# Kernel tuning notes

Measured on AMD Instinct MI355X. Metric: run time of the kernel, lower is better.

## Reference

```python
import jax, jax.numpy as jnp
import numpy as np


def setup_inputs() -> dict:
    key = jax.random.key(0)
    k1, k2, k3, k4 = jax.random.split(key, 4)
    B, T, C, H = 4, 2048, 1024, 64
    x = jax.random.normal(k1, (B, T, C), dtype=jnp.float32)
    # Linear(embed_dim, head_size, bias=False) weights, stored as [C, H] for x @ W
    s = 1.0 / np.sqrt(C)
    Wq = jax.random.normal(k2, (C, H), dtype=jnp.float32) * s
    Wk = jax.random.normal(k3, (C, H), dtype=jnp.float32) * s
    Wv = jax.random.normal(k4, (C, H), dtype=jnp.float32) * s
    return {"x": x, "Wq": Wq, "Wk": Wk, "Wv": Wv}


def reference(x, Wq, Wk, Wv):
    B, T, C = x.shape
    q = x @ Wq  # [B, T, H]
    k = x @ Wk
    v = x @ Wv
    # NOTE: original scales by embed_dim**-0.5 (C), not head_size**-0.5
    scale = C ** (-0.5)
    wei = jnp.einsum("bqh,bkh->bqk", q, k) * scale  # [B, T, T]
    causal = jnp.tril(jnp.ones((T, T), dtype=bool))
    wei = jnp.where(causal, wei, -jnp.inf)
    wei = jax.nn.softmax(wei, axis=-1)
    # dropout_rate = 0 -> identity
    out = jnp.einsum("bqk,bkh->bqh", wei, v)  # [B, T, H]
    return out
```

## Files before the change

### kernel.cpp

```cpp
#include <hip/hip_runtime.h>
#include <hip/hip_bf16.h>
#include <cmath>

#define B_ 4
#define T_ 2048
#define C_ 1024
#define H_ 64
#define K2_ 0.04508422003f
#define THRRAW_ 177.0f
#define NEG_ -3.0e38f

typedef __attribute__((ext_vector_type(4))) float f32x4;
typedef __attribute__((ext_vector_type(8))) short s16x8;
typedef __attribute__((ext_vector_type(4))) unsigned short u16x4;
typedef __attribute__((ext_vector_type(8))) unsigned short u16x8;

__device__ inline unsigned short f2bf(float f) {
    union { __hip_bfloat16 h; unsigned short u; } cv;
    cv.h = __float2bfloat16(f);
    return cv.u;
}

#define LDK 72

__global__ __launch_bounds__(256) void wprep(
    const float* __restrict__ Wq, const float* __restrict__ Wk,
    const float* __restrict__ Wv, unsigned short* __restrict__ wt)
{
    const int g = blockIdx.x * 256 + threadIdx.x;
    const int c = g >> 7;
    const int kg = (g & 127) * 8;
    const float* W = (c < 64) ? Wq : (c < 128) ? Wk : Wv;
    const int col = c & 63;
    u16x4 a, b;
    a.x = f2bf(W[(size_t)(kg + 0) * H_ + col]);
    a.y = f2bf(W[(size_t)(kg + 1) * H_ + col]);
    a.z = f2bf(W[(size_t)(kg + 2) * H_ + col]);
    a.w = f2bf(W[(size_t)(kg + 3) * H_ + col]);
    b.x = f2bf(W[(size_t)(kg + 4) * H_ + col]);
    b.y = f2bf(W[(size_t)(kg + 5) * H_ + col]);
    b.z = f2bf(W[(size_t)(kg + 6) * H_ + col]);
    b.w = f2bf(W[(size_t)(kg + 7) * H_ + col]);
    *(u16x4*)&wt[(size_t)c * C_ + kg] = a;
    *(u16x4*)&wt[(size_t)c * C_ + kg + 4] = b;
}

__global__ __launch_bounds__(256, 4) void proj_dbuf(
    const float* __restrict__ x, const unsigned short* __restrict__ wt,
    unsigned short* __restrict__ qb, unsigned short* __restrict__ kb,
    unsigned short* __restrict__ vt)
{
    __shared__ alignas(16) unsigned short As[2][64 * LDK];
    __shared__ alignas(16) unsigned short Bs[2][64 * LDK];

    const int t = threadIdx.x, lane = t & 63, w = t >> 6;
    const int blk = blockIdx.x;
    const int mat = blk % 3;
    const int row0 = (blk / 3) * 64;
    const int wr = (w >> 1) * 32, wc = (w & 1) * 32;
    const int fr = lane & 15, ko = (lane >> 4) * 8;

    const int ar0 = t >> 4, akc = (t & 15) * 4;
    const int bc0 = t >> 3, bkc = (t & 7) * 8;

    const float* xp = x + (size_t)(row0 + ar0) * C_ + akc;
    const unsigned short* wp = wt + (size_t)(mat * 64 + bc0) * C_ + bkc;

    f32x4 pa[4];
    u16x8 pb[2];

    #pragma unroll
    for (int i = 0; i < 4; ++i) pa[i] = *(const f32x4*)(xp + (size_t)i * 16 * C_);
    #pragma unroll
    for (int i = 0; i < 2; ++i) pb[i] = *(const u16x8*)(wp + (size_t)i * 32 * C_);
    #pragma unroll
    for (int i = 0; i < 4; ++i) {
        u16x4 bv;
        bv.x = f2bf(pa[i].x); bv.y = f2bf(pa[i].y);
        bv.z = f2bf(pa[i].z); bv.w = f2bf(pa[i].w);
        *(u16x4*)&As[0][(ar0 + i * 16) * LDK + akc] = bv;
    }
    #pragma unroll
    for (int i = 0; i < 2; ++i)
        *(u16x8*)&Bs[0][(bc0 + i * 32) * LDK + bkc] = pb[i];

    f32x4 acc[2][2];
    #pragma unroll
    for (int mi = 0; mi < 2; ++mi)
        #pragma unroll
        for (int ni = 0; ni < 2; ++ni)
            acc[mi][ni] = (f32x4){0.f, 0.f, 0.f, 0.f};

    for (int it = 0; it < 16; ++it) {
        __syncthreads();
        const int cur = it & 1;
        if (it < 15) {
            const float* xn = xp + (it + 1) * 64;
            const unsigned short* wn = wp + (it + 1) * 64;
            #pragma unroll
            for (int i = 0; i < 4; ++i) pa[i] = *(const f32x4*)(xn + (size_t)i * 16 * C_);
            #pragma unroll
            for (int i = 0; i < 2; ++i) pb[i] = *(const u16x8*)(wn + (size_t)i * 32 * C_);
        }
        const unsigned short* A = &As[cur][0];
        const unsigned short* Bb = &Bs[cur][0];
        #pragma unroll
        for (int ks = 0; ks < 2; ++ks) {
            s16x8 a0 = *(const s16x8*)&A[(wr + fr) * LDK + ks * 32 + ko];
            s16x8 a1 = *(const s16x8*)&A[(wr + 16 + fr) * LDK + ks * 32 + ko];
            s16x8 b0 = *(const s16x8*)&Bb[(wc + fr) * LDK + ks * 32 + ko];
            s16x8 b1 = *(const s16x8*)&Bb[(wc + 16 + fr) * LDK + ks * 32 + ko];
            acc[0][0] = __builtin_amdgcn_mfma_f32_16x16x32_bf16(a0, b0, acc[0][0], 0, 0, 0);
            acc[0][1] = __builtin_amdgcn_mfma_f32_16x16x32_bf16(a0, b1, acc[0][1], 0, 0, 0);
            acc[1][0] = __builtin_amdgcn_mfma_f32_16x16x32_bf16(a1, b0, acc[1][0], 0, 0, 0);
            acc[1][1] = __builtin_amdgcn_mfma_f32_16x16x32_bf16(a1, b1, acc[1][1], 0, 0, 0);
        }
        if (it < 15) {
            const int nxt = cur ^ 1;
            #pragma unroll
            for (int i = 0; i < 4; ++i) {
                u16x4 bv;
                bv.x = f2bf(pa[i].x); bv.y = f2bf(pa[i].y);
                bv.z = f2bf(pa[i].z); bv.w = f2bf(pa[i].w);
                *(u16x4*)&As[nxt][(ar0 + i * 16) * LDK + akc] = bv;
            }
            #pragma unroll
            for (int i = 0; i < 2; ++i)
                *(u16x8*)&Bs[nxt][(bc0 + i * 32) * LDK + bkc] = pb[i];
        }
    }

    if (mat < 2) {
        unsigned short* outb = (mat == 0) ? qb : kb;
        #pragma unroll
        for (int mi = 0; mi < 2; ++mi)
            #pragma unroll
            for (int ni = 0; ni < 2; ++ni)
                #pragma unroll
                for (int j = 0; j < 4; ++j) {
                    int row = row0 + wr + mi * 16 + (lane >> 4) * 4 + j;
                    int col = wc + ni * 16 + fr;
                    outb[(size_t)row * H_ + col] = f2bf(acc[mi][ni][j]);
                }
    } else {
        __syncthreads();
        unsigned short* Tr = &As[0][0];
        #pragma unroll
        for (int mi = 0; mi < 2; ++mi)
            #pragma unroll
            for (int ni = 0; ni < 2; ++ni)
                #pragma unroll
                for (int j = 0; j < 4; ++j) {
                    int r = wr + mi * 16 + (lane >> 4) * 4 + j;
                    int cc = wc + ni * 16 + fr;
                    Tr[cc * LDK + r] = f2bf(acc[mi][ni][j]);
                }
        __syncthreads();
        int h = t >> 2, c0 = (t & 3) * 16;
        int bb = row0 >> 11, trow = row0 & 2047;
        s16x8 v0 = *(const s16x8*)&Tr[h * LDK + c0];
        s16x8 v1 = *(const s16x8*)&Tr[h * LDK + c0 + 8];
        size_t dst = (size_t)bb * H_ * T_ + (size_t)h * T_ + trow + c0;
        *(s16x8*)&vt[dst] = v0;
        *(s16x8*)&vt[dst + 8] = v1;
    }
}

__global__ __launch_bounds__(512, 4) void attn_mfma(
    const unsigned short* __restrict__ qb, const unsigned short* __restrict__ kb,
    const unsigned short* __restrict__ vt, float* __restrict__ out)
{
    __shared__ alignas(16) unsigned short Ps[8][1024];
    __shared__ float Os[8][16][68];
    __shared__ float Mm[8][16];
    __shared__ float Ll[8][16];

    const int t = threadIdx.x, lane = t & 63, w = t >> 6;
    const int fr = lane & 15, hi4 = lane >> 4;
    const int blk = blockIdx.x;
    const int b = blk & 3;
    const int qt = 127 - (blk >> 2);
    const int qbase = qt * 16;

    const unsigned short* qp = qb + ((size_t)b * T_ + qbase) * H_;
    const unsigned short* kp = kb + (size_t)b * T_ * H_;
    const unsigned short* vp = vt + (size_t)b * H_ * T_;

    s16x8 qf0 = *(const s16x8*)&qp[fr * H_ + hi4 * 8];
    s16x8 qf1 = *(const s16x8*)&qp[fr * H_ + 32 + hi4 * 8];

    const int nt = (qbase + 79) >> 6;
    const int per = (nt + 7) >> 3;
    const int tb = w * per;
    int te = tb + per; if (te > nt) te = nt;

    float m = NEG_, l = 0.f;
    f32x4 o[4];
    #pragma unroll
    for (int hf = 0; hf < 4; ++hf) o[hf] = (f32x4){0.f, 0.f, 0.f, 0.f};

    unsigned short* P = &Ps[w][0];
    const int swz = (fr & 3) << 4;
    const int qrow = qbase + fr;

    for (int kt = tb; kt < te; ++kt) {
        const int kt0 = kt << 6;

        f32x4 s[4];
        #pragma unroll
        for (int n = 0; n < 4; ++n) {
            const unsigned short* kr = &kp[(size_t)(kt0 + n * 16 + fr) * H_ + hi4 * 8];
            s16x8 kf0 = *(const s16x8*)kr;
            s16x8 kf1 = *(const s16x8*)(kr + 32);
            f32x4 a = (f32x4){0.f, 0.f, 0.f, 0.f};
            a = __builtin_amdgcn_mfma_f32_16x16x32_bf16(kf0, qf0, a, 0, 0, 0);
            a = __builtin_amdgcn_mfma_f32_16x16x32_bf16(kf1, qf1, a, 0, 0, 0);
            s[n] = a;
        }

        s16x8 vf[4][2];
        #pragma unroll
        for (int hf = 0; hf < 4; ++hf) {
            const unsigned short* vr = &vp[(size_t)(hf * 16 + fr) * T_ + kt0 + hi4 * 8];
            vf[hf][0] = *(const s16x8*)vr;
            vf[hf][1] = *(const s16x8*)(vr + 32);
        }

        if (kt0 + 63 > qbase) {
            #pragma unroll
            for (int n = 0; n < 4; ++n)
                #pragma unroll
                for (int j = 0; j < 4; ++j) {
                    int key = kt0 + n * 16 + hi4 * 4 + j;
                    s[n][j] = (key > qrow) ? NEG_ : s[n][j];
                }
        }

        float mxl = fmaxf(fmaxf(fmaxf(fmaxf(s[0][0], s[0][1]), fmaxf(s[0][2], s[0][3])),
                                fmaxf(fmaxf(s[1][0], s[1][1]), fmaxf(s[1][2], s[1][3]))),
                          fmaxf(fmaxf(fmaxf(s[2][0], s[2][1]), fmaxf(s[2][2], s[2][3])),
                                fmaxf(fmaxf(s[3][0], s[3][1]), fmaxf(s[3][2], s[3][3]))));
        if (!__all(mxl - m <= THRRAW_)) {
            float mx = fmaxf(mxl, __shfl_xor(mxl, 16));
            mx = fmaxf(mx, __shfl_xor(mx, 32));
            float mn = fmaxf(m, mx);
            float corr = exp2f((m - mn) * K2_);
            m = mn;
            l *= corr;
            #pragma unroll
            for (int j = 0; j < 4; ++j) {
                float cj = __shfl(corr, (lane & 48) + hi4 * 4 + j);
                o[0][j] *= cj; o[1][j] *= cj; o[2][j] *= cj; o[3][j] *= cj;
            }
        }
        const float nmk = -m * K2_;
        float sum = 0.f;
        #pragma unroll
        for (int n = 0; n < 4; ++n)
            #pragma unroll
            for (int j = 0; j < 4; ++j) {
                float p = exp2f(fmaf(s[n][j], K2_, nmk));
                s[n][j] = p; sum += p;
            }
        sum += __shfl_xor(sum, 16);
        sum += __shfl_xor(sum, 32);
        l += sum;

        #pragma unroll
        for (int n = 0; n < 4; ++n) {
            u16x4 pk;
            pk.x = f2bf(s[n][0]); pk.y = f2bf(s[n][1]);
            pk.z = f2bf(s[n][2]); pk.w = f2bf(s[n][3]);
            *(u16x4*)&P[fr * 64 + ((n * 16 + hi4 * 4) ^ swz)] = pk;
        }
        s16x8 pa0 = *(const s16x8*)&P[fr * 64 + ((hi4 * 8) ^ swz)];
        s16x8 pa1 = *(const s16x8*)&P[fr * 64 + ((32 + hi4 * 8) ^ swz)];

        #pragma unroll
        for (int hf = 0; hf < 4; ++hf) {
            o[hf] = __builtin_amdgcn_mfma_f32_16x16x32_bf16(pa0, vf[hf][0], o[hf], 0, 0, 0);
            o[hf] = __builtin_amdgcn_mfma_f32_16x16x32_bf16(pa1, vf[hf][1], o[hf], 0, 0, 0);
        }
    }

    if (hi4 == 0) { Mm[w][fr] = m; Ll[w][fr] = l; }
    #pragma unroll
    for (int hf = 0; hf < 4; ++hf)
        #pragma unroll
        for (int j = 0; j < 4; ++j)
            Os[w][hi4 * 4 + j][hf * 16 + fr] = o[hf][j];
    __syncthreads();

    if (t < 256) {
        int qq = t >> 4, h0 = (t & 15) * 4;
        float M = NEG_;
        #pragma unroll
        for (int s8 = 0; s8 < 8; ++s8) M = fmaxf(M, Mm[s8][qq]);
        float L = 0.f;
        f32x4 r = (f32x4){0.f, 0.f, 0.f, 0.f};
        #pragma unroll
        for (int s8 = 0; s8 < 8; ++s8) {
            float e = exp2f((Mm[s8][qq] - M) * K2_);
            L += Ll[s8][qq] * e;
            f32x4 osv = *(const f32x4*)&Os[s8][qq][h0];
            r.x = fmaf(osv.x, e, r.x);
            r.y = fmaf(osv.y, e, r.y);
            r.z = fmaf(osv.z, e, r.z);
            r.w = fmaf(osv.w, e, r.w);
        }
        float il = 1.0f / L;
        r.x *= il; r.y *= il; r.z *= il; r.w *= il;
        *(f32x4*)&out[((size_t)b * T_ + qbase + qq) * H_ + h0] = r;
    }
}

extern "C" void kernel_launch(void* const* d_in, const int* in_sizes, int n_in,
                              void* d_out, int out_size, void* d_ws, size_t ws_size,
                              hipStream_t stream) {
    const float* x  = (const float*)d_in[0];
    const float* Wq = (const float*)d_in[1];
    const float* Wk = (const float*)d_in[2];
    const float* Wv = (const float*)d_in[3];
    float* outp = (float*)d_out;

    unsigned short* base = (unsigned short*)d_ws;
    unsigned short* qbw = base;
    unsigned short* kbw = base + 524288;
    unsigned short* vtw = base + 1048576;
    unsigned short* wtw = base + 1572864;

    wprep<<<96, 256, 0, stream>>>(Wq, Wk, Wv, wtw);
    proj_dbuf<<<(B_ * T_ / 64) * 3, 256, 0, stream>>>(x, wtw, qbw, kbw, vtw);
    attn_mfma<<<B_ * (T_ / 16), 512, 0, stream>>>(qbw, kbw, vtw, outp);
}
```

Baseline: 50.20 us.

## Split attention KV range across 16 waves per block with shared LDS union

New measurement: 79.05 us. 57.5% more time.

```diff
diff --git a/kernel.cpp b/kernel.cpp
--- a/kernel.cpp
+++ b/kernel.cpp
@@ -166,14 +166,13 @@
     }
 }
 
-__global__ __launch_bounds__(512, 4) void attn_mfma(
+__global__ __launch_bounds__(1024, 8) void attn_mfma(
     const unsigned short* __restrict__ qb, const unsigned short* __restrict__ kb,
     const unsigned short* __restrict__ vt, float* __restrict__ out)
 {
-    __shared__ alignas(16) unsigned short Ps[8][1024];
-    __shared__ float Os[8][16][68];
-    __shared__ float Mm[8][16];
-    __shared__ float Ll[8][16];
+    __shared__ alignas(16) unsigned char UB[69632];
+    __shared__ float Mm[16][16];
+    __shared__ float Ll[16][16];
 
     const int t = threadIdx.x, lane = t & 63, w = t >> 6;
     const int fr = lane & 15, hi4 = lane >> 4;
@@ -190,7 +189,7 @@
     s16x8 qf1 = *(const s16x8*)&qp[fr * H_ + 32 + hi4 * 8];
 
     const int nt = (qbase + 79) >> 6;
-    const int per = (nt + 7) >> 3;
+    const int per = (nt + 15) >> 4;
     const int tb = w * per;
     int te = tb + per; if (te > nt) te = nt;
 
@@ -199,17 +198,24 @@
     #pragma unroll
     for (int hf = 0; hf < 4; ++hf) o[hf] = (f32x4){0.f, 0.f, 0.f, 0.f};
 
-    unsigned short* P = &Ps[w][0];
+    unsigned short* P = (unsigned short*)UB + w * 1152;
     const int swz = (fr & 3) << 4;
     const int qrow = qbase + fr;
 
+    const unsigned short* kp0 = kp + (size_t)tb * 4096 + fr * H_ + hi4 * 8;
+    const unsigned short* kp2 = kp0 + 2048;
+    const unsigned short* vq0 = vp + (size_t)(fr) * T_      + tb * 64 + hi4 * 8;
+    const unsigned short* vq1 = vp + (size_t)(16 + fr) * T_ + tb * 64 + hi4 * 8;
+    const unsigned short* vq2 = vp + (size_t)(32 + fr) * T_ + tb * 64 + hi4 * 8;
+    const unsigned short* vq3 = vp + (size_t)(48 + fr) * T_ + tb * 64 + hi4 * 8;
+
     for (int kt = tb; kt < te; ++kt) {
         const int kt0 = kt << 6;
 
         f32x4 s[4];
         #pragma unroll
         for (int n = 0; n < 4; ++n) {
-            const unsigned short* kr = &kp[(size_t)(kt0 + n * 16 + fr) * H_ + hi4 * 8];
+            const unsigned short* kr = ((n < 2) ? kp0 : kp2) + (n & 1) * 1024;
             s16x8 kf0 = *(const s16x8*)kr;
             s16x8 kf1 = *(const s16x8*)(kr + 32);
             f32x4 a = (f32x4){0.f, 0.f, 0.f, 0.f};
@@ -218,13 +224,13 @@
             s[n] = a;
         }
 
-        s16x8 vf[4][2];
-        #pragma unroll
-        for (int hf = 0; hf < 4; ++hf) {
-            const unsigned short* vr = &vp[(size_t)(hf * 16 + fr) * T_ + kt0 + hi4 * 8];
-            vf[hf][0] = *(const s16x8*)vr;
-            vf[hf][1] = *(const s16x8*)(vr + 32);
-        }
+        s16x8 vf0a = *(const s16x8*)vq0, vf0b = *(const s16x8*)(vq0 + 32);
+        s16x8 vf1a = *(const s16x8*)vq1, vf1b = *(const s16x8*)(vq1 + 32);
+        s16x8 vf2a = *(const s16x8*)vq2, vf2b = *(const s16x8*)(vq2 + 32);
+        s16x8 vf3a = *(const s16x8*)vq3, vf3b = *(const s16x8*)(vq3 + 32);
+
+        kp0 += 4096; kp2 += 4096;
+        vq0 += 64; vq1 += 64; vq2 += 64; vq3 += 64;
 
         if (kt0 + 63 > qbase) {
             #pragma unroll
@@ -271,38 +277,43 @@
             u16x4 pk;
             pk.x = f2bf(s[n][0]); pk.y = f2bf(s[n][1]);
             pk.z = f2bf(s[n][2]); pk.w = f2bf(s[n][3]);
-            *(u16x4*)&P[fr * 64 + ((n * 16 + hi4 * 4) ^ swz)] = pk;
-        }
-        s16x8 pa0 = *(const s16x8*)&P[fr * 64 + ((hi4 * 8) ^ swz)];
-        s16x8 pa1 = *(const s16x8*)&P[fr * 64 + ((32 + hi4 * 8) ^ swz)];
-
-        #pragma unroll
-        for (int hf = 0; hf < 4; ++hf) {
-            o[hf] = __builtin_amdgcn_mfma_f32_16x16x32_bf16(pa0, vf[hf][0], o[hf], 0, 0, 0);
-            o[hf] = __builtin_amdgcn_mfma_f32_16x16x32_bf16(pa1, vf[hf][1], o[hf], 0, 0, 0);
-        }
-    }
-
+            *(u16x4*)&P[fr * 72 + ((n * 16 + hi4 * 4) ^ swz)] = pk;
+        }
+        s16x8 pa0 = *(const s16x8*)&P[fr * 72 + ((hi4 * 8) ^ swz)];
+        s16x8 pa1 = *(const s16x8*)&P[fr * 72 + ((32 + hi4 * 8) ^ swz)];
+
+        o[0] = __builtin_amdgcn_mfma_f32_16x16x32_bf16(pa0, vf0a, o[0], 0, 0, 0);
+        o[0] = __builtin_amdgcn_mfma_f32_16x16x32_bf16(pa1, vf0b, o[0], 0, 0, 0);
+        o[1] = __builtin_amdgcn_mfma_f32_16x16x32_bf16(pa0, vf1a, o[1], 0, 0, 0);
+        o[1] = __builtin_amdgcn_mfma_f32_16x16x32_bf16(pa1, vf1b, o[1], 0, 0, 0);
+        o[2] = __builtin_amdgcn_mfma_f32_16x16x32_bf16(pa0, vf2a, o[2], 0, 0, 0);
+        o[2] = __builtin_amdgcn_mfma_f32_16x16x32_bf16(pa1, vf2b, o[2], 0, 0, 0);
+        o[3] = __builtin_amdgcn_mfma_f32_16x16x32_bf16(pa0, vf3a, o[3], 0, 0, 0);
+        o[3] = __builtin_amdgcn_mfma_f32_16x16x32_bf16(pa1, vf3b, o[3], 0, 0, 0);
+    }
+
+    __syncthreads();
+    float* Ob = (float*)UB;
     if (hi4 == 0) { Mm[w][fr] = m; Ll[w][fr] = l; }
     #pragma unroll
     for (int hf = 0; hf < 4; ++hf)
         #pragma unroll
         for (int j = 0; j < 4; ++j)
-            Os[w][hi4 * 4 + j][hf * 16 + fr] = o[hf][j];
+            Ob[((size_t)w * 16 + hi4 * 4 + j) * 68 + hf * 16 + fr] = o[hf][j];
     __syncthreads();
 
     if (t < 256) {
         int qq = t >> 4, h0 = (t & 15) * 4;
         float M = NEG_;
         #pragma unroll
-        for (int s8 = 0; s8 < 8; ++s8) M = fmaxf(M, Mm[s8][qq]);
+        for (int s16_ = 0; s16_ < 16; ++s16_) M = fmaxf(M, Mm[s16_][qq]);
         float L = 0.f;
         f32x4 r = (f32x4){0.f, 0.f, 0.f, 0.f};
         #pragma unroll
-        for (int s8 = 0; s8 < 8; ++s8) {
-            float e = exp2f((Mm[s8][qq] - M) * K2_);
-            L += Ll[s8][qq] * e;
-            f32x4 osv = *(const f32x4*)&Os[s8][qq][h0];
+        for (int s16_ = 0; s16_ < 16; ++s16_) {
+            float e = exp2f((Mm[s16_][qq] - M) * K2_);
+            L += Ll[s16_][qq] * e;
+            f32x4 osv = *(const f32x4*)&Ob[((size_t)s16_ * 16 + qq) * 68 + h0];
             r.x = fmaf(osv.x, e, r.x);
             r.y = fmaf(osv.y, e, r.y);
             r.z = fmaf(osv.z, e, r.z);
@@ -331,5 +342,5 @@
 
     wprep<<<96, 256, 0, stream>>>(Wq, Wk, Wv, wtw);
     proj_dbuf<<<(B_ * T_ / 64) * 3, 256, 0, stream>>>(x, wtw, qbw, kbw, vtw);
-    attn_mfma<<<B_ * (T_ / 16), 512, 0, stream>>>(qbw, kbw, vtw, outp);
-}
+    attn_mfma<<<B_ * (T_ / 16), 1024, 0, stream>>>(qbw, kbw, vtw, outp);
+}
```
